# Performance work log

Measured on AMD Instinct MI355X. Metric: run time of the kernel, lower is better.

## Reference

```python
import jax, jax.numpy as jnp
import numpy as np
from jax import lax

# Module dims (match init_kwargs / input_specs)
CIN, COUT, K, STRIDE = 8, 16, 3, 2
U = V = 32                      # input spatial size (inshape = (CIN, U, V))
UO = VO = U // STRIDE           # 'same' padding with stride -> 16
IN_DIM = CIN * U * V + 1        # 8193 (homogeneous)
OUT_DIM = COUT * UO * VO + 1    # 4097 (homogeneous)
N = 1024                        # batch (columns of x_affine)


def setup_inputs() -> dict:
    key = jax.random.key(0)
    k1, k2, k3, k4, k5 = jax.random.split(key, 5)
    w = jax.random.normal(k1, (COUT, CIN, K, K), dtype=jnp.float32) * 0.1
    b = jax.random.normal(k2, (COUT,), dtype=jnp.float32) * 0.1
    # Keying matrices (dense stand-ins for the sparse keys); scaled to keep values sane.
    A = jax.random.normal(k3, (OUT_DIM, OUT_DIM), dtype=jnp.float32) / np.sqrt(OUT_DIM)
    Ainv = jax.random.normal(k4, (IN_DIM, IN_DIM), dtype=jnp.float32) / np.sqrt(IN_DIM)
    x_affine = jax.random.normal(k5, (IN_DIM, N), dtype=jnp.float32)
    return {"w": w, "b": b, "A": A, "Ainv": Ainv, "x_affine": x_affine}


def _toeplitz_conv_apply(z, w, b):
    """Apply the affine Toeplitz conv matrix T to z of shape (CIN*U*V+1, N).
    T = [[conv, bias], [0, 1]] so T@z = [conv(z[:-1]) + b*z[-1]; z[-1]]."""
    n = z.shape[1]
    hom = z[-1]                                   # (N,) homogeneous row
    x = z[:-1].T.reshape(n, CIN, U, V)            # (N, CIN, U, V)
    y = lax.conv_general_dilated(
        x, w, window_strides=(STRIDE, STRIDE), padding="SAME",
        dimension_numbers=("NCHW", "OIHW", "NCHW"))  # (N, COUT, UO, VO)
    y = y + b[None, :, None, None] * hom[:, None, None, None]
    yf = y.reshape(n, COUT * UO * VO).T           # (COUT*UO*VO, N)
    return jnp.concatenate([yf, hom[None, :]], axis=0)  # (OUT_DIM, N)


def reference(w, b, A, Ainv, x_affine):
    # What @ x = A @ T @ Ainv @ x  (factored; never materializes What)
    z = Ainv @ x_affine                # (IN_DIM, N)
    t = _toeplitz_conv_apply(z, w, b)  # (OUT_DIM, N)
    return A @ t                       # (OUT_DIM, N)
```

## Files before the change

kernel.cpp:

```cpp
#include <hip/hip_runtime.h>

#define IN_DIM 8193
#define OUT_DIM 4097
#define NB 1024
#define M1 8192
#define KP1 8256
#define M2 4096
#define KP2 4160

typedef __attribute__((ext_vector_type(8))) short short8;
typedef __attribute__((ext_vector_type(4))) float f32x4;

__device__ __forceinline__ unsigned short f2bf(float f) {
  unsigned int u = __float_as_uint(f);
  u = (u + 0x7fffu + ((u >> 16) & 1u)) >> 16;
  return (unsigned short)u;
}
__device__ __forceinline__ float bf2f(unsigned short u) {
  return __uint_as_float(((unsigned int)u) << 16);
}

__global__ __launch_bounds__(256) void cvt_pad_kernel(
    const float* __restrict__ src, unsigned short* __restrict__ dst,
    int sR, int sC, int dR, int dC) {
  int gid = blockIdx.x * 256 + threadIdx.x;
  int i4 = gid * 4;
  if (i4 >= dR * dC) return;
  int r = i4 / dC;
  int c = i4 - r * dC;
  unsigned short o[4];
#pragma unroll
  for (int j = 0; j < 4; ++j) {
    int cc = c + j;
    float v = (r < sR && cc < sC) ? src[(size_t)r * sC + cc] : 0.f;
    o[j] = f2bf(v);
  }
  unsigned int lo = (unsigned)o[0] | ((unsigned)o[1] << 16);
  unsigned int hi = (unsigned)o[2] | ((unsigned)o[3] << 16);
  *reinterpret_cast<uint2*>(dst + i4) = make_uint2(lo, hi);
}

__global__ __launch_bounds__(256) void transpose_cvt_zh_kernel(
    const float* __restrict__ src, unsigned short* __restrict__ dst,
    const float* __restrict__ arow, float* __restrict__ zh,
    int K, int N, int Kp) {
  __shared__ float tl[32][33];
  const int ntk = Kp >> 5;
  int bx = blockIdx.x % ntk;
  int by = blockIdx.x / ntk;
  int k0 = bx * 32, n0 = by * 32;
  int tx = threadIdx.x & 31, ty = threadIdx.x >> 5;
#pragma unroll
  for (int i = 0; i < 4; ++i) {
    int k = k0 + ty + i * 8;
    tl[ty + i * 8][tx] = (k < K) ? src[(size_t)k * N + n0 + tx] : 0.f;
  }
  const float av = (k0 + tx < K) ? arow[k0 + tx] : 0.f;
  __syncthreads();
#pragma unroll
  for (int i = 0; i < 4; ++i) {
    int n = n0 + ty + i * 8;
    float v = tl[tx][ty + i * 8];
    dst[(size_t)n * Kp + k0 + tx] = f2bf(v);
    float c = av * v;
#pragma unroll
    for (int m = 1; m <= 16; m <<= 1) c += __shfl_xor(c, m);
    if (tx == 0) atomicAdd(&zh[n], c);
  }
}

__global__ __launch_bounds__(256) void zero_kernel(float4* __restrict__ p, int n) {
  int i = blockIdx.x * 256 + threadIdx.x;
  if (i < n) p[i] = make_float4(0.f, 0.f, 0.f, 0.f);
}

template <int NKT, int NSPLIT, int BMBITS, int MROWS>
__global__ __launch_bounds__(512) void gemm_dp(
    const unsigned short* __restrict__ Ab,
    const unsigned short* __restrict__ Bt,
    float* __restrict__ C, int Kp) {
  extern __shared__ unsigned short lds[];
  const int tid = threadIdx.x;
  const int wid = tid >> 6;
  const int lane = tid & 63;
  const int b = blockIdx.x;
  const int x = b & 7, q = b >> 3;
  const int bm = (q & ((1 << BMBITS) - 1)) * 8 + x;
  const int bn = (q >> BMBITS) & 3;
  const int sp = q >> (BMBITS + 2);
  const int wm = (wid >> 2) << 7;
  const int wn = (wid & 3) << 6;

  const int qk = NKT / NSPLIT, rrk = NKT % NSPLIT;
  const int kt0 = sp * qk + (sp < rrk ? sp : rrk);
  const int T = qk + (sp < rrk ? 1 : 0);
  float* Cp = C + (size_t)sp * MROWS * NB;

  const int g0 = ((lane >> 4) ^ (lane & 7)) * 8;
  const int g1 = ((4 + (lane >> 4)) ^ (lane & 7)) * 8;
  const int alo = (lane & 15) * 64;
  const int bhalf = (wn >> 7) << 1;
  const int ahalf = (wid >> 2) << 1;
  const int bsub = ((wn & 64) << 6) + alo;

#define STAGEH(TT, ISA, H)                                                     \
  do {                                                                         \
    const int tt_ = (TT);                                                      \
    const int kc_ = kt0 + (tt_ < T - 1 ? tt_ : T - 1);                         \
    const int par_ = tt_ & 1;                                                  \
    const unsigned short* M_ = (ISA) ? Ab : Bt;                                \
    const int br_ = ((ISA) ? bm : bn) << 8;                                    \
    _Pragma("unroll")                                                          \
    for (int L_ = 0; L_ < 2; ++L_) {                                           \
      const int s_ = L_ * 512 + tid;                                           \
      const int row_ = s_ >> 3;                                                \
      const int gl_ = (s_ & 7) ^ (row_ & 7);                                   \
      const unsigned short* g_ = M_ + (size_t)(br_ + ((H) << 7) + row_) * Kp   \
                                    + (kc_ << 6) + gl_ * 8;                    \
      unsigned short* l_ = lds + (((ISA) ? 0 : 4) + ((H) << 1) + par_) * 8192  \
                               + (size_t)(L_ * 512 + wid * 64) * 8;            \
      __builtin_amdgcn_global_load_lds(                                        \
          (const __attribute__((address_space(1))) void*)g_,                   \
          (__attribute__((address_space(3))) void*)l_, 16, 0, 0);              \
    }                                                                          \
  } while (0)

#define MFMA16(BV0, BV1, NF0, NF1)                                             \
  do {                                                                         \
    __builtin_amdgcn_s_setprio(1);                                             \
    _Pragma("unroll")                                                          \
    for (int mf_ = 0; mf_ < 8; ++mf_) {                                        \
      asm volatile("v_mfma_f32_16x16x32_bf16 %0, %1, %2, %0"                   \
                   : "+v"(acc[mf_][NF0]) : "v"(af[mf_]), "v"(BV0));            \
      asm volatile("v_mfma_f32_16x16x32_bf16 %0, %1, %2, %0"                   \
                   : "+v"(acc[mf_][NF1]) : "v"(af[mf_]), "v"(BV1));            \
    }                                                                          \
    __builtin_amdgcn_s_setprio(0);                                             \
  } while (0)

#define PHASE_SYNC()                                                           \
  do {                                                                         \
    __builtin_amdgcn_s_barrier();                                              \
    asm volatile("s_waitcnt lgkmcnt(0)" ::: "memory");                         \
    __builtin_amdgcn_sched_barrier(0);                                         \
  } while (0)

  f32x4 acc[8][4];
#pragma unroll
  for (int i = 0; i < 8; ++i)
#pragma unroll
    for (int j = 0; j < 4; ++j) acc[i][j] = (f32x4)(0.0f);

  STAGEH(0, 1, 0); STAGEH(0, 1, 1);
  STAGEH(0, 0, 0); STAGEH(0, 0, 1);
  STAGEH(1, 1, 0); STAGEH(1, 1, 1);
  asm volatile("s_waitcnt vmcnt(4)" ::: "memory");
  __builtin_amdgcn_s_barrier();

  for (int t = 0; t < T; ++t) {
    const int par = t & 1;
    const unsigned short* Ab_ = lds + (ahalf + par) * 8192 + alo;
    const unsigned short* Bb_ = lds + (4 + bhalf + par) * 8192 + bsub;
    short8 af[8], b0, b1;
    STAGEH(t + 1, 0, 0);
#pragma unroll
    for (int mf = 0; mf < 8; ++mf)
      af[mf] = *reinterpret_cast<const short8*>(Ab_ + mf * 1024 + g0);
    b0 = *reinterpret_cast<const short8*>(Bb_ + 0 * 1024 + g0);
    b1 = *reinterpret_cast<const short8*>(Bb_ + 1 * 1024 + g0);
    PHASE_SYNC();
    MFMA16(b0, b1, 0, 1);
    __builtin_amdgcn_s_barrier();
    STAGEH(t + 1, 0, 1);
    b0 = *reinterpret_cast<const short8*>(Bb_ + 2 * 1024 + g0);
    b1 = *reinterpret_cast<const short8*>(Bb_ + 3 * 1024 + g0);
    PHASE_SYNC();
    MFMA16(b0, b1, 2, 3);
    __builtin_amdgcn_s_barrier();
#pragma unroll
    for (int mf = 0; mf < 8; ++mf)
      af[mf] = *reinterpret_cast<const short8*>(Ab_ + mf * 1024 + g1);
    b0 = *reinterpret_cast<const short8*>(Bb_ + 2 * 1024 + g1);
    b1 = *reinterpret_cast<const short8*>(Bb_ + 3 * 1024 + g1);
    PHASE_SYNC();
    MFMA16(b0, b1, 2, 3);
    __builtin_amdgcn_s_barrier();
    STAGEH(t + 2, 1, 0); STAGEH(t + 2, 1, 1);
    b0 = *reinterpret_cast<const short8*>(Bb_ + 0 * 1024 + g1);
    b1 = *reinterpret_cast<const short8*>(Bb_ + 1 * 1024 + g1);
    asm volatile("s_waitcnt vmcnt(4)" ::: "memory");
    PHASE_SYNC();
    MFMA16(b0, b1, 0, 1);
    __builtin_amdgcn_s_barrier();
  }
#undef STAGEH
#undef MFMA16
#undef PHASE_SYNC

#pragma unroll
  for (int mf = 0; mf < 8; ++mf) {
    const int rb = (bm << 8) + wm + mf * 16 + ((lane >> 4) << 2);
#pragma unroll
    for (int nf = 0; nf < 4; ++nf) {
      const int col = (bn << 8) + wn + nf * 16 + (lane & 15);
#pragma unroll
      for (int r = 0; r < 4; ++r)
        Cp[(size_t)(rb + r) * NB + col] = acc[mf][nf][r];
    }
  }
}

__global__ __launch_bounds__(256) void conv_lds_kernel(
    const float* __restrict__ za, const float* __restrict__ zb,
    const float* __restrict__ zh, const float* __restrict__ w,
    const float* __restrict__ bias, unsigned short* __restrict__ tT) {
  __shared__ float zl[24 * 18 * 32];
  __shared__ float wl[1152];
  __shared__ float bl[16];
  const int b = blockIdx.x;
  const int nt = b & 31, vh = (b >> 5) & 1, uo = b >> 6;
  const int n0 = nt * 32;
  const int tid = threadIdx.x;
#pragma unroll
  for (int it = 0; it < 5; ++it) {
    const int idx = it * 256 + tid;
    if (idx < 1152) wl[idx] = w[idx];
  }
  if (tid < 16) bl[tid] = bias[tid];
  const int nl4 = (tid & 7) * 4;
#pragma unroll
  for (int it = 0; it < 13; ++it) {
    const int R = it * 32 + (tid >> 3);
    if (R < 408) {
      const int ci = R / 51;
      const int rem = R - ci * 51;
      const int kh = rem / 17;
      const int vi = rem - kh * 17;
      const int u = 2 * uo + kh;
      const int v = vh * 16 + vi;
      float4 val = make_float4(0.f, 0.f, 0.f, 0.f);
      if (u < 32 && v < 32) {
        const size_t g = ((size_t)(ci * 1024 + u * 32 + v)) * 1024 + n0 + nl4;
        const float4 a4 = *reinterpret_cast<const float4*>(za + g);
        const float4 b4 = *reinterpret_cast<const float4*>(zb + g);
        val = make_float4(a4.x + b4.x, a4.y + b4.y, a4.z + b4.z, a4.w + b4.w);
      }
      *reinterpret_cast<float4*>(zl + ((ci * 3 + kh) * 18 + vi) * 32 + nl4) = val;
    }
  }
  __syncthreads();
  const int nl = tid & 31;
  const int cop = tid >> 5;
  const float hom = zh[n0 + nl];
  float acc[2][8];
#pragma unroll
  for (int c = 0; c < 2; ++c) {
    const float bb = bl[cop + c * 8] * hom;
#pragma unroll
    for (int vo = 0; vo < 8; ++vo) acc[c][vo] = bb;
  }
  for (int ci = 0; ci < 8; ++ci) {
#pragma unroll
    for (int kh = 0; kh < 3; ++kh) {
      const float* zr = zl + (ci * 3 + kh) * (18 * 32) + nl;
      float zv[17];
#pragma unroll
      for (int vi = 0; vi < 17; ++vi) zv[vi] = zr[vi * 32];
#pragma unroll
      for (int c = 0; c < 2; ++c) {
        const int co = cop + c * 8;
        const float* wp = wl + ((co * 8 + ci) * 3 + kh) * 3;
#pragma unroll
        for (int kw = 0; kw < 3; ++kw) {
          const float wv = wp[kw];
#pragma unroll
          for (int vo = 0; vo < 8; ++vo) acc[c][vo] += wv * zv[2 * vo + kw];
        }
      }
    }
  }
#pragma unroll
  for (int c = 0; c < 2; ++c) {
    const int co = cop + c * 8;
    unsigned short o[8];
#pragma unroll
    for (int vo = 0; vo < 8; ++vo) o[vo] = f2bf(acc[c][vo]);
    uint4 pv;
    pv.x = (unsigned)o[0] | ((unsigned)o[1] << 16);
    pv.y = (unsigned)o[2] | ((unsigned)o[3] << 16);
    pv.z = (unsigned)o[4] | ((unsigned)o[5] << 16);
    pv.w = (unsigned)o[6] | ((unsigned)o[7] << 16);
    *reinterpret_cast<uint4*>(
        tT + (size_t)(n0 + nl) * KP2 + co * 256 + uo * 16 + vh * 8) = pv;
  }
}

__global__ __launch_bounds__(256) void homrow_kernel(
    const float* __restrict__ zh, unsigned short* __restrict__ tT) {
  const int n = blockIdx.x * 256 + threadIdx.x;
  unsigned short* p = tT + (size_t)n * KP2 + 4096;
  uint4 z4 = make_uint4(0u, 0u, 0u, 0u);
  uint4 h4 = z4;
  h4.x = (unsigned)f2bf(zh[n]);
  *reinterpret_cast<uint4*>(p) = h4;
#pragma unroll
  for (int i = 1; i < 8; ++i) *reinterpret_cast<uint4*>(p + i * 8) = z4;
}

__global__ __launch_bounds__(256) void sum4_kernel(
    const float* __restrict__ p, float* __restrict__ out, int n4) {
  const int i = blockIdx.x * 256 + threadIdx.x;
  if (i >= n4) return;
  const size_t stride4 = (size_t)M2 * NB / 4;
  const float4* p4 = (const float4*)p;
  float4 a = p4[i];
  float4 b = p4[i + stride4];
  float4 c = p4[i + 2 * stride4];
  float4 d = p4[i + 3 * stride4];
  float4 r;
  r.x = (a.x + b.x) + (c.x + d.x);
  r.y = (a.y + b.y) + (c.y + d.y);
  r.z = (a.z + b.z) + (c.z + d.z);
  r.w = (a.w + b.w) + (c.w + d.w);
  reinterpret_cast<float4*>(out)[i] = r;
}

__global__ __launch_bounds__(256) void outrow_kernel(
    const unsigned short* __restrict__ A2row,
    const unsigned short* __restrict__ tT, float* __restrict__ out) {
  const int wid = threadIdx.x >> 6, lane = threadIdx.x & 63;
  const int n = blockIdx.x * 4 + wid;
  const unsigned short* trow = tT + (size_t)n * KP2;
  float acc = 0.f;
#pragma unroll
  for (int it = 0; it < 9; ++it) {
    const int i8 = it * 64 + lane;
    if (i8 < KP2 / 8) {
      short8 tv = *reinterpret_cast<const short8*>(trow + i8 * 8);
      short8 av = *reinterpret_cast<const short8*>(A2row + i8 * 8);
#pragma unroll
      for (int j = 0; j < 8; ++j)
        acc += bf2f((unsigned short)tv[j]) * bf2f((unsigned short)av[j]);
    }
  }
#pragma unroll
  for (int m = 1; m <= 32; m <<= 1) acc += __shfl_xor(acc, m);
  if (lane == 0) out[(size_t)4096 * NB + n] = acc;
}

extern "C" void kernel_launch(void* const* d_in, const int* in_sizes, int n_in,
                              void* d_out, int out_size, void* d_ws, size_t ws_size,
                              hipStream_t stream) {
  const float* w    = (const float*)d_in[0];
  const float* bias = (const float*)d_in[1];
  const float* A    = (const float*)d_in[2];
  const float* Ainv = (const float*)d_in[3];
  const float* x    = (const float*)d_in[4];
  float* out = (float*)d_out;

  char* ws = (char*)d_ws;
  const size_t o_xT = (size_t)M1 * KP1 * 2;
  const size_t o_z2 = o_xT + (size_t)NB * KP1 * 2;
  const size_t o_tT = o_z2 + (size_t)2 * M1 * NB * 4;
  const size_t o_zh = o_tT + (size_t)NB * KP2 * 2;
  unsigned short* Ainv_b = (unsigned short*)ws;
  unsigned short* xT_b   = (unsigned short*)(ws + o_xT);
  float*          z2     = (float*)(ws + o_z2);
  unsigned short* tT_b   = (unsigned short*)(ws + o_tT);
  float*          zh     = (float*)(ws + o_zh);
  unsigned short* A2_b   = (unsigned short*)ws;
  float*          outp   = (float*)(ws + (size_t)OUT_DIM * KP2 * 2);
  (void)ws_size; (void)in_sizes; (void)n_in; (void)out_size;

  hipFuncSetAttribute((const void*)gemm_dp<129, 2, 2, M1>,
                      hipFuncAttributeMaxDynamicSharedMemorySize, 131072);
  hipFuncSetAttribute((const void*)gemm_dp<65, 4, 1, M2>,
                      hipFuncAttributeMaxDynamicSharedMemorySize, 131072);

  zero_kernel<<<1, 256, 0, stream>>>((float4*)zh, 256);
  cvt_pad_kernel<<<(M1 * KP1 / 4) / 256, 256, 0, stream>>>(
      Ainv, Ainv_b, IN_DIM, IN_DIM, M1, KP1);
  transpose_cvt_zh_kernel<<<(KP1 / 32) * (NB / 32), 256, 0, stream>>>(
      x, xT_b, Ainv + (size_t)8192 * IN_DIM, zh, IN_DIM, NB, KP1);
  gemm_dp<129, 2, 2, M1><<<256, 512, 131072, stream>>>(
      Ainv_b, xT_b, z2, KP1);
  conv_lds_kernel<<<1024, 256, 0, stream>>>(
      z2, z2 + (size_t)M1 * NB, zh, w, bias, tT_b);
  homrow_kernel<<<4, 256, 0, stream>>>(zh, tT_b);
  cvt_pad_kernel<<<(OUT_DIM * KP2 / 4 + 255) / 256, 256, 0, stream>>>(
      A, A2_b, OUT_DIM, OUT_DIM, OUT_DIM, KP2);
  gemm_dp<65, 4, 1, M2><<<256, 512, 131072, stream>>>(
      A2_b, tT_b, outp, KP2);
  sum4_kernel<<<(M2 * NB / 4) / 256, 256, 0, stream>>>(
      outp, out, M2 * NB / 4);
  outrow_kernel<<<NB / 4, 256, 0, stream>>>(
      A2_b + (size_t)4096 * KP2, tT_b, out);
}
```

Baseline: 422.4 us.

## Fold conv and bias into Ainv to halve first GEMM rows

Precomputes W4 = T_conv·Ainv (4096 x 8193) directly from Ainv and the conv weights, so the first GEMM produces the conv output with M=4096 instead of computing z with M=8192 and then convolving. This removes the Ainv bf16 conversion, halves the first GEMM's FLOPs, and replaces the conv kernel with a split-K sum plus transpose. In exchange it adds a W4 build kernel that reads up to 9 strided Ainv rows per output row in fp32 (about 36 reads per Ainv element), and it changes where bf16 rounding happens.

```diff
diff --git a/kernel.cpp b/kernel.cpp
--- a/kernel.cpp
+++ b/kernel.cpp
@@ -3,7 +3,6 @@
 #define IN_DIM 8193
 #define OUT_DIM 4097
 #define NB 1024
-#define M1 8192
 #define KP1 8256
 #define M2 4096
 #define KP2 4160
@@ -72,6 +71,57 @@
 __global__ __launch_bounds__(256) void zero_kernel(float4* __restrict__ p, int n) {
   int i = blockIdx.x * 256 + threadIdx.x;
   if (i < n) p[i] = make_float4(0.f, 0.f, 0.f, 0.f);
+}
+
+__global__ __launch_bounds__(256) void w4_build_kernel(
+    const float* __restrict__ Ainv, const float* __restrict__ w,
+    const float* __restrict__ bias, unsigned short* __restrict__ W4) {
+  __shared__ float wl[1152];
+  __shared__ float bl[16];
+  const int b = blockIdx.x;
+  const int cq = b & 3;
+  const int uv = b >> 2;
+  const int uo = uv >> 4, vo = uv & 15;
+  const int tid = threadIdx.x;
+#pragma unroll
+  for (int it = 0; it < 5; ++it) {
+    const int i = it * 256 + tid;
+    if (i < 1152) wl[i] = w[i];
+  }
+  if (tid < 16) bl[tid] = bias[tid];
+  __syncthreads();
+  const int c0 = cq * 2064, c1 = c0 + 2064;
+  for (int cc = c0; cc < c1; cc += 256) {
+    const int c = cc + tid;
+    if (c >= c1) break;
+    float acc[16];
+    const float hv = (c < IN_DIM) ? Ainv[(size_t)8192 * IN_DIM + c] : 0.f;
+#pragma unroll
+    for (int co = 0; co < 16; ++co) acc[co] = bl[co] * hv;
+    if (c < IN_DIM) {
+      for (int ci = 0; ci < 8; ++ci) {
+#pragma unroll
+        for (int kh = 0; kh < 3; ++kh) {
+          const int u = 2 * uo + kh;
+          if (u >= 32) continue;
+#pragma unroll
+          for (int kw = 0; kw < 3; ++kw) {
+            const int v = 2 * vo + kw;
+            if (v >= 32) continue;
+            const float a = Ainv[(size_t)(ci * 1024 + u * 32 + v) * IN_DIM + c];
+            const float* wp = wl + (ci * 3 + kh) * 3 + kw;
+#pragma unroll
+            for (int co = 0; co < 16; ++co) acc[co] += wp[co * 72] * a;
+          }
+        }
+      }
+    }
+    const int r0 = uo * 16 + vo;
+#pragma unroll
+    for (int co = 0; co < 16; ++co)
+      W4[(size_t)(co * 256 + r0) * KP1 + c] =
+          f2bf((c < IN_DIM) ? acc[co] : 0.f);
+  }
 }
 
 template <int NKT, int NSPLIT, int BMBITS, int MROWS>
@@ -210,88 +260,26 @@
   }
 }
 
-__global__ __launch_bounds__(256) void conv_lds_kernel(
-    const float* __restrict__ za, const float* __restrict__ zb,
-    const float* __restrict__ zh, const float* __restrict__ w,
-    const float* __restrict__ bias, unsigned short* __restrict__ tT) {
-  __shared__ float zl[24 * 18 * 32];
-  __shared__ float wl[1152];
-  __shared__ float bl[16];
-  const int b = blockIdx.x;
-  const int nt = b & 31, vh = (b >> 5) & 1, uo = b >> 6;
-  const int n0 = nt * 32;
-  const int tid = threadIdx.x;
-#pragma unroll
-  for (int it = 0; it < 5; ++it) {
-    const int idx = it * 256 + tid;
-    if (idx < 1152) wl[idx] = w[idx];
-  }
-  if (tid < 16) bl[tid] = bias[tid];
-  const int nl4 = (tid & 7) * 4;
-#pragma unroll
-  for (int it = 0; it < 13; ++it) {
-    const int R = it * 32 + (tid >> 3);
-    if (R < 408) {
-      const int ci = R / 51;
-      const int rem = R - ci * 51;
-      const int kh = rem / 17;
-      const int vi = rem - kh * 17;
-      const int u = 2 * uo + kh;
-      const int v = vh * 16 + vi;
-      float4 val = make_float4(0.f, 0.f, 0.f, 0.f);
-      if (u < 32 && v < 32) {
-        const size_t g = ((size_t)(ci * 1024 + u * 32 + v)) * 1024 + n0 + nl4;
-        const float4 a4 = *reinterpret_cast<const float4*>(za + g);
-        const float4 b4 = *reinterpret_cast<const float4*>(zb + g);
-        val = make_float4(a4.x + b4.x, a4.y + b4.y, a4.z + b4.z, a4.w + b4.w);
-      }
-      *reinterpret_cast<float4*>(zl + ((ci * 3 + kh) * 18 + vi) * 32 + nl4) = val;
-    }
+__global__ __launch_bounds__(256) void sum4t_kernel(
+    const float* __restrict__ tp, unsigned short* __restrict__ tT) {
+  __shared__ float tl[32][33];
+  const int nr = M2 / 32;
+  const int br = blockIdx.x % nr;
+  const int bn = blockIdx.x / nr;
+  const int r0 = br * 32, n0 = bn * 32;
+  const int tx = threadIdx.x & 31, ty = threadIdx.x >> 5;
+  const size_t S = (size_t)M2 * NB;
+#pragma unroll
+  for (int i = 0; i < 4; ++i) {
+    const int r = r0 + ty + i * 8;
+    const size_t g = (size_t)r * NB + n0 + tx;
+    tl[ty + i * 8][tx] = (tp[g] + tp[g + S]) + (tp[g + 2 * S] + tp[g + 3 * S]);
   }
   __syncthreads();
-  const int nl = tid & 31;
-  const int cop = tid >> 5;
-  const float hom = zh[n0 + nl];
-  float acc[2][8];
-#pragma unroll
-  for (int c = 0; c < 2; ++c) {
-    const float bb = bl[cop + c * 8] * hom;
-#pragma unroll
-    for (int vo = 0; vo < 8; ++vo) acc[c][vo] = bb;
-  }
-  for (int ci = 0; ci < 8; ++ci) {
-#pragma unroll
-    for (int kh = 0; kh < 3; ++kh) {
-      const float* zr = zl + (ci * 3 + kh) * (18 * 32) + nl;
-      float zv[17];
-#pragma unroll
-      for (int vi = 0; vi < 17; ++vi) zv[vi] = zr[vi * 32];
-#pragma unroll
-      for (int c = 0; c < 2; ++c) {
-        const int co = cop + c * 8;
-        const float* wp = wl + ((co * 8 + ci) * 3 + kh) * 3;
-#pragma unroll
-        for (int kw = 0; kw < 3; ++kw) {
-          const float wv = wp[kw];
-#pragma unroll
-          for (int vo = 0; vo < 8; ++vo) acc[c][vo] += wv * zv[2 * vo + kw];
-        }
-      }
-    }
-  }
-#pragma unroll
-  for (int c = 0; c < 2; ++c) {
-    const int co = cop + c * 8;
-    unsigned short o[8];
-#pragma unroll
-    for (int vo = 0; vo < 8; ++vo) o[vo] = f2bf(acc[c][vo]);
-    uint4 pv;
-    pv.x = (unsigned)o[0] | ((unsigned)o[1] << 16);
-    pv.y = (unsigned)o[2] | ((unsigned)o[3] << 16);
-    pv.z = (unsigned)o[4] | ((unsigned)o[5] << 16);
-    pv.w = (unsigned)o[6] | ((unsigned)o[7] << 16);
-    *reinterpret_cast<uint4*>(
-        tT + (size_t)(n0 + nl) * KP2 + co * 256 + uo * 16 + vh * 8) = pv;
+#pragma unroll
+  for (int i = 0; i < 4; ++i) {
+    const int n = n0 + ty + i * 8;
+    tT[(size_t)n * KP2 + r0 + tx] = f2bf(tl[tx][ty + i * 8]);
   }
 }
 
@@ -359,33 +347,31 @@
   float* out = (float*)d_out;
 
   char* ws = (char*)d_ws;
-  const size_t o_xT = (size_t)M1 * KP1 * 2;
-  const size_t o_z2 = o_xT + (size_t)NB * KP1 * 2;
-  const size_t o_tT = o_z2 + (size_t)2 * M1 * NB * 4;
+  const size_t o_xT = (size_t)M2 * KP1 * 2;
+  const size_t o_tp = o_xT + (size_t)NB * KP1 * 2;
+  const size_t o_tT = o_tp + (size_t)4 * M2 * NB * 4;
   const size_t o_zh = o_tT + (size_t)NB * KP2 * 2;
-  unsigned short* Ainv_b = (unsigned short*)ws;
-  unsigned short* xT_b   = (unsigned short*)(ws + o_xT);
-  float*          z2     = (float*)(ws + o_z2);
-  unsigned short* tT_b   = (unsigned short*)(ws + o_tT);
-  float*          zh     = (float*)(ws + o_zh);
-  unsigned short* A2_b   = (unsigned short*)ws;
-  float*          outp   = (float*)(ws + (size_t)OUT_DIM * KP2 * 2);
+  unsigned short* W4   = (unsigned short*)ws;
+  unsigned short* xT_b = (unsigned short*)(ws + o_xT);
+  float*          tp   = (float*)(ws + o_tp);
+  unsigned short* tT_b = (unsigned short*)(ws + o_tT);
+  float*          zh   = (float*)(ws + o_zh);
+  unsigned short* A2_b = (unsigned short*)(ws + o_tp);
+  float*          outp = (float*)ws;
   (void)ws_size; (void)in_sizes; (void)n_in; (void)out_size;
 
-  hipFuncSetAttribute((const void*)gemm_dp<129, 2, 2, M1>,
+  hipFuncSetAttribute((const void*)gemm_dp<129, 4, 1, M2>,
                       hipFuncAttributeMaxDynamicSharedMemorySize, 131072);
   hipFuncSetAttribute((const void*)gemm_dp<65, 4, 1, M2>,
                       hipFuncAttributeMaxDynamicSharedMemorySize, 131072);
 
   zero_kernel<<<1, 256, 0, stream>>>((float4*)zh, 256);
-  cvt_pad_kernel<<<(M1 * KP1 / 4) / 256, 256, 0, stream>>>(
-      Ainv, Ainv_b, IN_DIM, IN_DIM, M1, KP1);
   transpose_cvt_zh_kernel<<<(KP1 / 32) * (NB / 32), 256, 0, stream>>>(
       x, xT_b, Ainv + (size_t)8192 * IN_DIM, zh, IN_DIM, NB, KP1);
-  gemm_dp<129, 2, 2, M1><<<256, 512, 131072, stream>>>(
-      Ainv_b, xT_b, z2, KP1);
-  conv_lds_kernel<<<1024, 256, 0, stream>>>(
-      z2, z2 + (size_t)M1 * NB, zh, w, bias, tT_b);
+  w4_build_kernel<<<1024, 256, 0, stream>>>(Ainv, w, bias, W4);
+  gemm_dp<129, 4, 1, M2><<<256, 512, 131072, stream>>>(
+      W4, xT_b, tp, KP1);
+  sum4t_kernel<<<(M2 / 32) * (NB / 32), 256, 0, stream>>>(tp, tT_b);
   homrow_kernel<<<4, 256, 0, stream>>>(zh, tT_b);
   cvt_pad_kernel<<<(OUT_DIM * KP2 / 4 + 255) / 256, 256, 0, stream>>>(
       A, A2_b, OUT_DIM, OUT_DIM, OUT_DIM, KP2);
```

Result: slower. 577.6 us (+36.7%).
